# Kernel tuning notes

Hardware: AMD Instinct MI355X
Metric: run time of the kernel (lower is better)

## Reference

```python
import jax, jax.numpy as jnp
import numpy as np

EPS = 1e-5


def setup_inputs() -> dict:
    key = jax.random.key(0)
    ks = jax.random.split(key, 8)
    g, p, d, h, w = 32, 64, 512, 24, 8
    hw = h * w
    return {
        "gal_fea": jax.random.normal(ks[0], (g, d, h, w), dtype=jnp.float32),
        "prob_fea": jax.random.normal(ks[1], (p, d, h, w), dtype=jnp.float32),
        "bn_weight": jnp.ones((1,), jnp.float32),
        "bn_bias": jnp.zeros((1,), jnp.float32),
        "bn_mean": jax.random.normal(ks[2], (1,), jnp.float32) * 0.1,
        "bn_var": jax.random.uniform(ks[3], (1,), jnp.float32, 0.5, 1.5),
        "fc_weight": jax.random.normal(ks[4], (1, 2 * hw), jnp.float32) * 0.05,
        "fc_bias": jnp.zeros((1,), jnp.float32),
        "lbn_weight": jnp.ones((1,), jnp.float32),
        "lbn_bias": jnp.zeros((1,), jnp.float32),
        "lbn_mean": jax.random.normal(ks[5], (1,), jnp.float32) * 0.1,
        "lbn_var": jax.random.uniform(ks[6], (1,), jnp.float32, 0.5, 1.5),
    }


def reference(gal_fea, prob_fea, bn_weight, bn_bias, bn_mean, bn_var,
              fc_weight, fc_bias, lbn_weight, lbn_bias, lbn_mean, lbn_var):
    g, d, h, w = gal_fea.shape
    p = prob_fea.shape[0]
    hw = h * w
    # 1x1 conv with probe pixels as kernels == batched correlation (QK^T style)
    gal = gal_fea.reshape(g, d, hw)                                  # [g, d, hw_x]
    ker = jnp.transpose(prob_fea, (0, 2, 3, 1)).reshape(p, hw, d)    # [p, hw_y, d]
    s = jnp.einsum('gdx,pyd->gpyx', gal, ker)                        # [g, p, hw_y, hw_x]
    # dual-axis max pooling, then concat: [g, p, 2*hw]
    score = jnp.concatenate([s.max(axis=2), s.max(axis=3)], axis=-1)
    # BatchNorm1d(1) in eval mode: scalar affine with running stats
    score = (score - bn_mean) * (bn_weight / jnp.sqrt(bn_var + EPS)) + bn_bias
    # fc: Linear(2*hw, 1)
    score = score.reshape(g * p, 2 * hw) @ fc_weight[0] + fc_bias[0]  # [g*p]
    score = score.reshape(g, p)
    # logit BatchNorm1d(1), eval mode
    score = (score - lbn_mean) * (lbn_weight / jnp.sqrt(lbn_var + EPS)) + lbn_bias
    return jax.nn.sigmoid(score / 10.0)
```

## Files before the change

### kernel.cpp

```cpp
#include <hip/hip_runtime.h>
#include <hip/hip_bf16.h>
#include <cstdint>
#include <cstddef>

#define NG 32
#define NP 64
#define ND 512
#define HW 192
#define KS 32
#define EPSV 1e-5f

typedef _Float16 half8 __attribute__((ext_vector_type(8)));
typedef float floatx4 __attribute__((ext_vector_type(4)));
typedef float floatx16 __attribute__((ext_vector_type(16)));

__global__ __launch_bounds__(256) void prep_frag(const float* __restrict__ gal,
                                                 const float* __restrict__ prob,
                                                 _Float16* __restrict__ galT4,
                                                 _Float16* __restrict__ probT4) {
  __shared__ float lds[16 * 192];
  const int z = blockIdx.x;
  const int ks = blockIdx.y;
  const float* src;
  _Float16* dst;
  if (z < NP) {
    src = prob + (size_t)z * ND * HW;
    dst = probT4 + (size_t)z * 98304;
  } else {
    src = gal + (size_t)(z - NP) * ND * HW;
    dst = galT4 + (size_t)(z - NP) * 98304;
  }
  src += (size_t)ks * 16 * HW;
  dst += (size_t)ks * 3072;
  const int t = threadIdx.x;
#pragma unroll
  for (int i = 0; i < 12; ++i) lds[i * 256 + t] = src[i * 256 + t];
  __syncthreads();
#pragma unroll
  for (int r = 0; r < 2; ++r) {
    const int h = r * 256 + t;
    if (h < 384) {
      const int rb = h >> 6, hi = (h >> 5) & 1, l31 = h & 31;
      half8 v;
#pragma unroll
      for (int j = 0; j < 8; ++j) v[j] = (_Float16)lds[(hi * 8 + j) * 192 + rb * 32 + l31];
      *(half8*)(dst + (size_t)h * 8) = v;
    }
  }
}

__device__ __forceinline__ void g2l16(const void* g, void* l) {
  __builtin_amdgcn_global_load_lds(
      (const __attribute__((address_space(1))) void*)g,
      (__attribute__((address_space(3))) void*)l, 16, 0, 0);
}

__global__ __launch_bounds__(256, 2) void qaconv_main(
    const _Float16* __restrict__ galT4, const _Float16* __restrict__ probT4,
    const float* __restrict__ bn_w, const float* __restrict__ bn_b,
    const float* __restrict__ bn_m, const float* __restrict__ bn_v,
    const float* __restrict__ fc_w, const float* __restrict__ fc_b,
    const float* __restrict__ lbn_w, const float* __restrict__ lbn_b,
    const float* __restrict__ lbn_m, const float* __restrict__ lbn_v,
    float* __restrict__ out) {
  __shared__ __align__(16) char shmem[73728];
  __shared__ float colp[2][HW];
  __shared__ float wsum[4];
  float(*rowbuf)[66] = (float(*)[66])shmem;

  const int bid = blockIdx.x;
  const int g = bid >> 6, p = bid & 63;

  const int t = threadIdx.x;
  const int lane = t & 63, wid = t >> 6;
  const int wr = wid & 1;
  const int wc = wid >> 1;
  const int l31 = lane & 31, hi = lane >> 5;

  const _Float16* pAl = probT4 + (size_t)p * 98304 + wid * 512 + lane * 8;
  const _Float16* pBl = galT4 + (size_t)g * 98304 + wid * 512 + lane * 8;
  const int sdst = wid * 1024;

  char* const b0 = shmem;
  char* const b1 = shmem + 24576;
  char* const b2 = shmem + 49152;

  floatx16 acc[3][3];
#pragma unroll
  for (int ii = 0; ii < 3; ++ii)
#pragma unroll
    for (int jj = 0; jj < 3; ++jj) acc[ii][jj] = (floatx16)0.f;

#define STAGE(kt_, base_)                                            \
  {                                                                  \
    char* db_ = (base_) + sdst;                                      \
    const _Float16* sa_ = pAl + (size_t)(kt_)*6144;                  \
    const _Float16* sb_ = pBl + (size_t)(kt_)*6144;                  \
    g2l16(sa_, db_);                                                 \
    g2l16(sa_ + 2048, db_ + 4096);                                   \
    g2l16(sa_ + 4096, db_ + 8192);                                   \
    g2l16(sb_, db_ + 12288);                                         \
    g2l16(sb_ + 2048, db_ + 16384);                                  \
    g2l16(sb_ + 4096, db_ + 20480);                                  \
  }

#define KC_BODY(base_, kc_)                                                      \
  {                                                                              \
    const char* bA_ = (base_) + (kc_)*6144;                                      \
    const char* bB_ = (base_) + 12288 + (kc_)*6144;                              \
    half8 af[3], bf[3];                                                          \
    _Pragma("unroll") for (int f = 0; f < 3; ++f) {                              \
      af[f] = *(const half8*)(bA_ + (wr * 3 + f) * 1024 + lane * 16);            \
      bf[f] = *(const half8*)(bB_ + (wc * 3 + f) * 1024 + lane * 16);            \
    }                                                                            \
    __builtin_amdgcn_s_setprio(1);                                               \
    _Pragma("unroll") for (int ii = 0; ii < 3; ++ii)                             \
        _Pragma("unroll") for (int jj = 0; jj < 3; ++jj)                         \
            acc[ii][jj] = __builtin_amdgcn_mfma_f32_32x32x16_f16(af[ii], bf[jj], \
                                                                 acc[ii][jj], 0, 0, 0); \
    __builtin_amdgcn_s_setprio(0);                                               \
  }

#define COMPUTE(base_) KC_BODY(base_, 0) KC_BODY(base_, 1)

#define SLOT(kt_, rdb_, stb_, doStage_)                  \
  {                                                      \
    asm volatile("s_waitcnt vmcnt(6)" ::: "memory");     \
    __builtin_amdgcn_s_barrier();                        \
    if (doStage_) STAGE((kt_) + 2, stb_)                 \
    COMPUTE(rdb_)                                        \
  }

  STAGE(0, b0)
  STAGE(1, b1)

#pragma unroll 1
  for (int m = 0; m < 5; ++m) {
    const int kt = m * 3;
    SLOT(kt + 0, b0, b2, true)
    SLOT(kt + 1, b1, b0, true)
    SLOT(kt + 2, b2, b1, (m < 4))
  }
  asm volatile("s_waitcnt vmcnt(0)" ::: "memory");
  __builtin_amdgcn_s_barrier();
  COMPUTE(b0)
#undef STAGE
#undef KC_BODY
#undef COMPUTE
#undef SLOT

#pragma unroll
  for (int fb = 0; fb < 3; ++fb) {
    float v = -3.4e38f;
#pragma unroll
    for (int fa = 0; fa < 3; ++fa)
#pragma unroll
      for (int e = 0; e < 16; ++e) v = fmaxf(v, acc[fa][fb][e]);
    v = fmaxf(v, __shfl_xor(v, 32));
    if (lane < 32) colp[wr][wc * 96 + fb * 32 + lane] = v;
  }
  __syncthreads();
#pragma unroll
  for (int fa = 0; fa < 3; ++fa)
#pragma unroll
    for (int e = 0; e < 16; ++e) {
      float rv = acc[fa][0][e];
      rv = fmaxf(rv, acc[fa][1][e]);
      rv = fmaxf(rv, acc[fa][2][e]);
      const int Y = wr * 96 + fa * 32 + (e & 3) + 8 * (e >> 2) + 4 * hi;
      rowbuf[Y][wc * 32 + l31] = rv;
    }
  __syncthreads();

  float partial = 0.f;
  if (t < HW) {
    const float* rb = rowbuf[t];
    float rmax = -3.4e38f;
#pragma unroll
    for (int j = 0; j < 16; ++j) {
      const floatx4 v = *(const floatx4*)&rb[j * 4];
      rmax = fmaxf(rmax, fmaxf(fmaxf(v[0], v[1]), fmaxf(v[2], v[3])));
    }
    const float cmax = fmaxf(colp[0][t], colp[1][t]);
    const float scale = bn_w[0] / sqrtf(bn_v[0] + EPSV);
    const float bm = bn_m[0], bb = bn_b[0];
    partial = ((cmax - bm) * scale + bb) * fc_w[t] +
              ((rmax - bm) * scale + bb) * fc_w[HW + t];
  }
#pragma unroll
  for (int off = 1; off < 64; off <<= 1) partial += __shfl_xor(partial, off);
  if (lane == 0) wsum[wid] = partial;
  __syncthreads();
  if (t == 0) {
    const float sum = fc_b[0] + wsum[0] + wsum[1] + wsum[2] + wsum[3];
    const float logit = (sum - lbn_m[0]) * (lbn_w[0] / sqrtf(lbn_v[0] + EPSV)) + lbn_b[0];
    out[bid] = 1.f / (1.f + expf(-logit * 0.1f));
  }
}

__global__ __launch_bounds__(256) void qaconv_naive(
    const float* __restrict__ gal, const float* __restrict__ prob,
    const float* __restrict__ bn_w, const float* __restrict__ bn_b,
    const float* __restrict__ bn_m, const float* __restrict__ bn_v,
    const float* __restrict__ fc_w, const float* __restrict__ fc_b,
    const float* __restrict__ lbn_w, const float* __restrict__ lbn_b,
    const float* __restrict__ lbn_m, const float* __restrict__ lbn_v,
    float* __restrict__ out) {
  __shared__ float prow[ND];
  __shared__ float rowmaxs[HW];
  __shared__ float colmaxs[HW];
  __shared__ float red[4];
  const int bid = blockIdx.x;
  const int g = bid >> 6, p = bid & 63;
  const int t = threadIdx.x, lane = t & 63, wid = t >> 6;
  const float* gp = gal + (size_t)g * ND * HW;
  const float* pp = prob + (size_t)p * ND * HW;
  float colmax = -3.4e38f;
  for (int y = 0; y < HW; ++y) {
    for (int k = t; k < ND; k += 256) prow[k] = pp[(size_t)k * HW + y];
    __syncthreads();
    float sv = -3.4e38f;
    if (t < HW) {
      sv = 0.f;
      for (int k = 0; k < ND; ++k) sv = fmaf(prow[k], gp[(size_t)k * HW + t], sv);
      colmax = fmaxf(colmax, sv);
    }
    float m = sv;
#pragma unroll
    for (int off = 1; off < 64; off <<= 1) m = fmaxf(m, __shfl_xor(m, off));
    if (lane == 0) red[wid] = m;
    __syncthreads();
    if (t == 0) rowmaxs[y] = fmaxf(fmaxf(red[0], red[1]), fmaxf(red[2], red[3]));
    __syncthreads();
  }
  if (t < HW) colmaxs[t] = colmax;
  __syncthreads();
  float partial = 0.f;
  for (int j = t; j < 2 * HW; j += 256) {
    const float v = (j < HW) ? colmaxs[j] : rowmaxs[j - HW];
    const float sc = (v - bn_m[0]) * (bn_w[0] / sqrtf(bn_v[0] + EPSV)) + bn_b[0];
    partial += sc * fc_w[j];
  }
#pragma unroll
  for (int off = 1; off < 64; off <<= 1) partial += __shfl_xor(partial, off);
  if (lane == 0) red[wid] = partial;
  __syncthreads();
  if (t == 0) {
    const float sum = fc_b[0] + red[0] + red[1] + red[2] + red[3];
    const float logit = (sum - lbn_m[0]) * (lbn_w[0] / sqrtf(lbn_v[0] + EPSV)) + lbn_b[0];
    out[bid] = 1.f / (1.f + expf(-logit * 0.1f));
  }
}

extern "C" void kernel_launch(void* const* d_in, const int* in_sizes, int n_in,
                              void* d_out, int out_size, void* d_ws, size_t ws_size,
                              hipStream_t stream) {
  const float* gal = (const float*)d_in[0];
  const float* prob = (const float*)d_in[1];
  const float* bn_w = (const float*)d_in[2];
  const float* bn_b = (const float*)d_in[3];
  const float* bn_m = (const float*)d_in[4];
  const float* bn_v = (const float*)d_in[5];
  const float* fc_w = (const float*)d_in[6];
  const float* fc_b = (const float*)d_in[7];
  const float* lbn_w = (const float*)d_in[8];
  const float* lbn_b = (const float*)d_in[9];
  const float* lbn_m = (const float*)d_in[10];
  const float* lbn_v = (const float*)d_in[11];
  float* out = (float*)d_out;

  const size_t probT4_elems = (size_t)NP * 98304;
  const size_t galT4_elems = (size_t)NG * 98304;
  const size_t ws_needed = (probT4_elems + galT4_elems) * sizeof(_Float16);
  if (ws_size >= ws_needed) {
    _Float16* probT4 = (_Float16*)d_ws;
    _Float16* galT4 = probT4 + probT4_elems;
    prep_frag<<<dim3(NP + NG, KS), dim3(256), 0, stream>>>(gal, prob, galT4, probT4);
    qaconv_main<<<dim3(NG * NP), dim3(256), 0, stream>>>(
        galT4, probT4, bn_w, bn_b, bn_m, bn_v, fc_w, fc_b, lbn_w, lbn_b, lbn_m, lbn_v, out);
  } else {
    qaconv_naive<<<dim3(NG * NP), dim3(256), 0, stream>>>(
        gal, prob, bn_w, bn_b, bn_m, bn_v, fc_w, fc_b, lbn_w, lbn_b, lbn_m, lbn_v, out);
  }
}
```

Before: 97.19 us.

## Restructure GEMM main loop into explicit read/stage/MFMA phases with sched barriers

```diff
diff --git a/kernel.cpp b/kernel.cpp
--- a/kernel.cpp
+++ b/kernel.cpp
@@ -91,6 +91,8 @@
 #pragma unroll
     for (int jj = 0; jj < 3; ++jj) acc[ii][jj] = (floatx16)0.f;
 
+  half8 raf[3], rbf[3];
+
 #define STAGE(kt_, base_)                                            \
   {                                                                  \
     char* db_ = (base_) + sdst;                                      \
@@ -104,49 +106,68 @@
     g2l16(sb_ + 4096, db_ + 20480);                                  \
   }
 
-#define KC_BODY(base_, kc_)                                                      \
+#define READ6(base_, kc_)                                            \
+  {                                                                  \
+    const char* bA_ = (base_) + (kc_)*6144;                          \
+    const char* bB_ = (base_) + 12288 + (kc_)*6144;                  \
+    raf[0] = *(const half8*)(bA_ + (wr * 3 + 0) * 1024 + lane * 16); \
+    raf[1] = *(const half8*)(bA_ + (wr * 3 + 1) * 1024 + lane * 16); \
+    raf[2] = *(const half8*)(bA_ + (wr * 3 + 2) * 1024 + lane * 16); \
+    rbf[0] = *(const half8*)(bB_ + (wc * 3 + 0) * 1024 + lane * 16); \
+    rbf[1] = *(const half8*)(bB_ + (wc * 3 + 1) * 1024 + lane * 16); \
+    rbf[2] = *(const half8*)(bB_ + (wc * 3 + 2) * 1024 + lane * 16); \
+  }
+
+#define MFMA9()                                                                  \
   {                                                                              \
-    const char* bA_ = (base_) + (kc_)*6144;                                      \
-    const char* bB_ = (base_) + 12288 + (kc_)*6144;                              \
-    half8 af[3], bf[3];                                                          \
-    _Pragma("unroll") for (int f = 0; f < 3; ++f) {                              \
-      af[f] = *(const half8*)(bA_ + (wr * 3 + f) * 1024 + lane * 16);            \
-      bf[f] = *(const half8*)(bB_ + (wc * 3 + f) * 1024 + lane * 16);            \
-    }                                                                            \
     __builtin_amdgcn_s_setprio(1);                                               \
     _Pragma("unroll") for (int ii = 0; ii < 3; ++ii)                             \
         _Pragma("unroll") for (int jj = 0; jj < 3; ++jj)                         \
-            acc[ii][jj] = __builtin_amdgcn_mfma_f32_32x32x16_f16(af[ii], bf[jj], \
+            acc[ii][jj] = __builtin_amdgcn_mfma_f32_32x32x16_f16(raf[ii], rbf[jj],\
                                                                  acc[ii][jj], 0, 0, 0); \
     __builtin_amdgcn_s_setprio(0);                                               \
   }
 
-#define COMPUTE(base_) KC_BODY(base_, 0) KC_BODY(base_, 1)
-
-#define SLOT(kt_, rdb_, stb_, doStage_)                  \
-  {                                                      \
-    asm volatile("s_waitcnt vmcnt(6)" ::: "memory");     \
-    __builtin_amdgcn_s_barrier();                        \
-    if (doStage_) STAGE((kt_) + 2, stb_)                 \
-    COMPUTE(rdb_)                                        \
+#define SLOT(kt_, rdb_, stb_, doStage_, vmW_)                        \
+  {                                                                  \
+                                                        \
+    READ6(rdb_, 0)                                                   \
+    if (doStage_) STAGE((kt_) + 2, stb_)                             \
+    __builtin_amdgcn_sched_barrier(0);                               \
+    __builtin_amdgcn_s_barrier();                                    \
+    asm volatile("s_waitcnt lgkmcnt(0)" ::: "memory");               \
+    __builtin_amdgcn_sched_barrier(0);                               \
+    MFMA9()                                                          \
+    __builtin_amdgcn_s_barrier();                                    \
+                                                        \
+    READ6(rdb_, 1)                                                   \
+    __builtin_amdgcn_sched_barrier(0);                               \
+    asm volatile("s_waitcnt vmcnt(" #vmW_ ")" ::: "memory");         \
+    __builtin_amdgcn_s_barrier();                                    \
+    asm volatile("s_waitcnt lgkmcnt(0)" ::: "memory");               \
+    __builtin_amdgcn_sched_barrier(0);                               \
+    MFMA9()                                                          \
+    __builtin_amdgcn_s_barrier();                                    \
   }
 
   STAGE(0, b0)
   STAGE(1, b1)
+  asm volatile("s_waitcnt vmcnt(6)" ::: "memory");
+  __builtin_amdgcn_s_barrier();
 
 #pragma unroll 1
-  for (int m = 0; m < 5; ++m) {
-    const int kt = m * 3;
-    SLOT(kt + 0, b0, b2, true)
-    SLOT(kt + 1, b1, b0, true)
-    SLOT(kt + 2, b2, b1, (m < 4))
-  }
-  asm volatile("s_waitcnt vmcnt(0)" ::: "memory");
-  __builtin_amdgcn_s_barrier();
-  COMPUTE(b0)
+  for (int m = 0; m < 4; ++m) {
+    SLOT(3 * m + 0, b0, b2, true, 6)
+    SLOT(3 * m + 1, b1, b0, true, 6)
+    SLOT(3 * m + 2, b2, b1, true, 6)
+  }
+  SLOT(12, b0, b2, true, 6)
+  SLOT(13, b1, b0, true, 6)
+  SLOT(14, b2, b1, false, 0)
+  SLOT(15, b0, b1, false, 0)
 #undef STAGE
-#undef KC_BODY
-#undef COMPUTE
+#undef READ6
+#undef MFMA9
 #undef SLOT
 
 #pragma unroll
```

Result: faster. 89.88 us, median of 2 (-7.5%).
